# Kernel optimization log

Hardware: AMD Instinct MI355X
Metric: run time of the kernel (lower is better)

The kernel has to match this reference:

```python
import jax, jax.numpy as jnp
import numpy as np

B, C, N, M = 4, 192, 160, 160
HEADS, DH = 4, 32
HID = HEADS * DH
NMEM = 4
SCALE = DH ** -0.5


def setup_inputs() -> dict:
    key = jax.random.key(0)
    ks = jax.random.split(key, 8)
    std = 0.05
    return {
        "x": jax.random.normal(ks[0], (B, C, N, M), jnp.float32),
        "gq": jnp.ones((C,), jnp.float32),
        "gk": jnp.ones((C,), jnp.float32),
        "gv": jnp.ones((C,), jnp.float32),
        "Wq": jax.random.normal(ks[1], (HID, C), jnp.float32) * std,
        "Wk": jax.random.normal(ks[2], (HID, C), jnp.float32) * std,
        "Wv": jax.random.normal(ks[3], (HID, C), jnp.float32) * std,
        "mem_kv": jax.random.normal(ks[4], (2, HEADS, NMEM, DH), jnp.float32),
        "Wo": jax.random.normal(ks[5], (C, HID), jnp.float32) * std,
        "bo": jnp.zeros((C,), jnp.float32),
        "Wr": jax.random.normal(ks[6], (C, 2 * C), jnp.float32) * std,
    }


def _rms(x, g):
    # lucidrains RMSNorm over channel axis 1: F.normalize(x, dim=1) * g * sqrt(dim)
    n = jnp.sqrt(jnp.sum(x * x, axis=1, keepdims=True))
    gshape = (1, -1) + (1,) * (x.ndim - 2)
    return x / jnp.maximum(n, 1e-12) * g.reshape(gshape) * jnp.sqrt(jnp.asarray(x.shape[1], x.dtype))


def _axial_attn(q_ft, k_ft, v_map, rep, Wq, Wk, Wv, mem_kv, Wo, bo, gq, gk, gv):
    # q_ft: (b, c, Lq) compact queries (spatial (1,Lq) in the original)
    # k_ft: (b, c, Lk) compact keys; original repeats them `rep` times -> (Lk*rep) keys
    # v_map: (b, c, Lk, rep) values (full map, not broadcast)
    # Exact math of softmax over [NMEM + Lk*rep] keys, exploiting the rep-fold
    # duplicated key scores so attn(key i, copy j) has identical weight p_i:
    #   out = sum_mem p_j mem_v_j + sum_i p_i * (sum_rep v[i, r])
    b = q_ft.shape[0]
    q = jnp.einsum('hdc,bcq->bhqd', Wq.reshape(HEADS, DH, -1), _rms(q_ft, gq))
    k = jnp.einsum('hdc,bck->bhkd', Wk.reshape(HEADS, DH, -1), _rms(k_ft, gk))
    v = jnp.einsum('hdc,bckr->bhkrd', Wv.reshape(HEADS, DH, -1), _rms(v_map, gv))
    v_sum = v.sum(axis=3)  # (b,h,Lk,d)
    mem_k, mem_v = mem_kv[0], mem_kv[1]
    s_k = jnp.einsum('bhqd,bhkd->bhqk', q, k) * SCALE      # (b,h,Lq,Lk)
    s_m = jnp.einsum('bhqd,hjd->bhqj', q, mem_k) * SCALE   # (b,h,Lq,NMEM)
    mx = jnp.maximum(s_k.max(-1), s_m.max(-1))             # (b,h,Lq)
    e_k = jnp.exp(s_k - mx[..., None])
    e_m = jnp.exp(s_m - mx[..., None])
    Z = e_m.sum(-1) + rep * e_k.sum(-1)                    # rep copies of each key
    out = (jnp.einsum('bhqj,hjd->bhqd', e_m, mem_v)
           + jnp.einsum('bhqk,bhkd->bhqd', e_k, v_sum)) / Z[..., None]
    out = out.transpose(0, 2, 1, 3).reshape(b, -1, HID)    # (b,Lq,hid), (h d) channel order
    return jnp.einsum('ck,bqk->bcq', Wo, out) + bo[None, :, None]  # (b,c,Lq)


def reference(x, gq, gk, gv, Wq, Wk, Wv, mem_kv, Wo, bo, Wr):
    # x: (b,c,n,m); mask=None path
    row_ft = x.mean(axis=3)  # (b,c,n)
    col_ft = x.mean(axis=2)  # (b,c,m)
    # row attention: n queries, keys = col_ft repeated n times, values = x^T (spatial (m,n))
    row_attn = _axial_attn(row_ft, col_ft, x.transpose(0, 1, 3, 2), N,
                           Wq, Wk, Wv, mem_kv, Wo, bo, gq, gk, gv)  # (b,c,n)
    # col attention (shared weights): m queries, keys = row_ft repeated m times, values = x
    col_attn = _axial_attn(col_ft, row_ft, x, M,
                           Wq, Wk, Wv, mem_kv, Wo, bo, gq, gk, gv)  # (b,c,m)
    # broadcast to (b,c,n,m), concat on channels, 1x1 conv reduce (bias=False)
    Wr1, Wr2 = Wr[:, :C], Wr[:, C:]
    out = (jnp.einsum('dc,bcn->bdn', Wr1, row_attn)[:, :, :, None]
           + jnp.einsum('dc,bcm->bdm', Wr2, col_attn)[:, :, None, :])
    return out
```

## Files before the change

kernel.cpp:

```cpp
#include <hip/hip_runtime.h>
#include <math.h>

constexpr int B_ = 4, C_ = 192, N_ = 160, M_ = 160;
constexpr int NM_ = N_ * M_;
constexpr float SQRT_C = 13.856406460551018f;
constexpr float SCALE_ = 0.17677669529663687f;

__device__ __forceinline__ float wred_sum(float v) {
    #pragma unroll
    for (int o = 32; o > 0; o >>= 1) v += __shfl_xor(v, o, 64);
    return v;
}
__device__ __forceinline__ float wred_max(float v) {
    #pragma unroll
    for (int o = 32; o > 0; o >>= 1) v = fmaxf(v, __shfl_xor(v, o, 64));
    return v;
}

__global__ void prep_kernel(const float* __restrict__ Wr, const float* __restrict__ Wo,
                            const float* __restrict__ bo,
                            const float* __restrict__ Wq, const float* __restrict__ Wk,
                            const float* __restrict__ Wv, const float* __restrict__ gq,
                            const float* __restrict__ gk, const float* __restrict__ gv,
                            float* __restrict__ WfT, float* __restrict__ bfb,
                            float* __restrict__ WT) {
    int bx = blockIdx.x, tid = threadIdx.x;
    if (bx < 192) {
        int sub = tid >> 7, hd = tid & 127;
        int pair = bx * 2 + sub;
        int t = pair / 192, dch = pair % 192;
        const float* wr = Wr + dch * 384 + t * 192;
        float acc = 0.f;
        for (int c = 0; c < 192; c++) acc += wr[c] * Wo[c * 128 + hd];
        WfT[hd * 384 + pair] = acc;
        if (hd == 0) {
            float s = 0.f;
            for (int c = 0; c < 192; c++) s += wr[c] * bo[c];
            bfb[pair] = s;
        }
    } else {
        int g = (bx - 192) * 256 + tid;
        int mat = g / 24576, r2 = g % 24576;
        int c = r2 >> 7, hd = r2 & 127;
        const float* W = (mat == 0) ? Wq : ((mat == 1) ? Wk : Wv);
        const float* gv_ = (mat == 0) ? gq : ((mat == 1) ? gk : gv);
        WT[g] = gv_[c] * W[hd * 192 + c];
    }
}

__global__ void ssq_part_kernel(const float* __restrict__ x, float* __restrict__ psum) {
    int bx = blockIdx.x;
    int chunk = bx / 400, blk = bx % 400;
    int g = blk * 256 + threadIdx.x;
    int b = g / NM_, nm = g - b * NM_;
    const float* xp = x + ((size_t)(b * C_ + chunk * 32)) * NM_ + nm;
    float ssq = 0.f;
    #pragma unroll
    for (int cc = 0; cc < 32; cc++) { float v = xp[(size_t)cc * NM_]; ssq += v * v; }
    psum[chunk * (B_ * NM_) + g] = ssq;
}

__global__ void rnorm_kernel(const float* __restrict__ psum, float* __restrict__ rn) {
    int g = blockIdx.x * 256 + threadIdx.x;
    float s = 0.f;
    #pragma unroll
    for (int ch = 0; ch < 6; ch++) s += psum[ch * (B_ * NM_) + g];
    rn[g] = SQRT_C / fmaxf(sqrtf(s), 1e-12f);
}

__global__ void rowcol_kernel(const float* __restrict__ x, const float* __restrict__ rn,
                              float* __restrict__ rowft, float* __restrict__ colft,
                              float* __restrict__ Srow, float* __restrict__ Scol) {
    __shared__ float cpart[8][2][160];
    int bc = blockIdx.x;
    int b = bc / C_;
    int tid = threadIdx.x, w = tid >> 6, lane = tid & 63;
    const float* xp = x + (size_t)bc * NM_;
    const float* rp = rn + (size_t)b * NM_;
    int m0 = lane, m1 = lane + 64, m2 = lane + 128;
    bool ok2 = (m2 < M_);
    float cr0 = 0, cr1 = 0, cr2 = 0, cn0 = 0, cn1 = 0, cn2 = 0;
    for (int n = w; n < N_; n += 8) {
        const float* xr = xp + n * M_;
        const float* rr = rp + n * M_;
        float a0 = xr[m0], a1 = xr[m1], a2 = ok2 ? xr[m2] : 0.f;
        float r0 = rr[m0], r1 = rr[m1], r2 = ok2 ? rr[m2] : 0.f;
        float b0 = a0 * r0, b1 = a1 * r1, b2 = a2 * r2;
        cr0 += a0; cr1 += a1; cr2 += a2;
        cn0 += b0; cn1 += b1; cn2 += b2;
        float rs = wred_sum(a0 + a1 + a2);
        float rsn = wred_sum(b0 + b1 + b2);
        if (lane == 0) {
            rowft[bc * N_ + n] = rs * (1.0f / 160.0f);
            Srow[bc * N_ + n] = rsn;
        }
    }
    cpart[w][0][m0] = cr0; cpart[w][0][m1] = cr1; if (ok2) cpart[w][0][m2] = cr2;
    cpart[w][1][m0] = cn0; cpart[w][1][m1] = cn1; if (ok2) cpart[w][1][m2] = cn2;
    __syncthreads();
    if (tid < M_) {
        float sr = 0.f, sn = 0.f;
        #pragma unroll
        for (int ww = 0; ww < 8; ww++) { sr += cpart[ww][0][tid]; sn += cpart[ww][1][tid]; }
        colft[bc * M_ + tid] = sr * (1.0f / 160.0f);
        Scol[bc * M_ + tid] = sn;
    }
}

__global__ void proj_kernel(const float* __restrict__ WT,
                            const float* __restrict__ rowft, const float* __restrict__ colft,
                            const float* __restrict__ Srow, const float* __restrict__ Scol,
                            float* __restrict__ Qb, float* __restrict__ Kb, float* __restrict__ Vb) {
    __shared__ float in_s[192 * 4];
    __shared__ float sc_s[4];
    int bx = blockIdx.x;
    int pt = bx % 40, rest = bx / 40;
    int mat = rest % 3; int r2 = rest / 3;
    int t = r2 % 2, b = r2 / 2;
    const float* src; float* dst;
    if (mat == 0)      { src = (t == 0) ? rowft : colft; dst = Qb; }
    else if (mat == 1) { src = (t == 0) ? colft : rowft; dst = Kb; }
    else               { src = (t == 0) ? Scol  : Srow;  dst = Vb; }
    const float* Wt = WT + mat * 24576;
    int tid = threadIdx.x;
    for (int idx = tid; idx < 192 * 4; idx += 256) {
        int c = idx >> 2, p = idx & 3;
        in_s[idx] = src[(b * C_ + c) * 160 + pt * 4 + p];
    }
    __syncthreads();
    int w = tid >> 6, lane = tid & 63;
    if (mat < 2) {
        float v0 = in_s[lane * 4 + w];
        float v1 = in_s[(lane + 64) * 4 + w];
        float v2 = in_s[(lane + 128) * 4 + w];
        float ssq = wred_sum(v0 * v0 + v1 * v1 + v2 * v2);
        if (lane == 0) sc_s[w] = SQRT_C / fmaxf(sqrtf(ssq), 1e-12f);
    } else {
        if (tid < 4) sc_s[tid] = 1.0f;
    }
    __syncthreads();
    int hd = tid & 127, pc = tid >> 7, p0 = pc * 2;
    float a0 = 0.f, a1 = 0.f;
    for (int c = 0; c < 192; c++) {
        float wv = Wt[c * 128 + hd];
        a0 += wv * in_s[c * 4 + p0];
        a1 += wv * in_s[c * 4 + p0 + 1];
    }
    int posbase = (b * 2 + t) * 160 + pt * 4 + p0;
    dst[(size_t)posbase * 128 + hd]       = a0 * sc_s[p0];
    dst[(size_t)(posbase + 1) * 128 + hd] = a1 * sc_s[p0 + 1];
}

__global__ void attn_kernel(const float* __restrict__ Qb, const float* __restrict__ Kb,
                            const float* __restrict__ Vb, const float* __restrict__ memkv,
                            float* __restrict__ AO) {
    __shared__ float k_s[160 * 33];
    __shared__ float v_s[160 * 33];
    __shared__ float q_s[8 * 33];
    __shared__ float e_s[8 * 160];
    __shared__ float mk[128];
    __shared__ float mv[128];
    int bx = blockIdx.x;
    int qt = bx % 20; int r = bx / 20;
    int h = r & 3; r >>= 2;
    int t = r & 1; int b = r >> 1;
    int tid = threadIdx.x, w = tid >> 6, lane = tid & 63;
    int btbase = ((b * 2 + t) * 160) * 128 + h * 32;
    for (int idx = tid; idx < 160 * 32; idx += 256) {
        int kk = idx >> 5, d = idx & 31;
        k_s[kk * 33 + d] = Kb[btbase + kk * 128 + d];
        v_s[kk * 33 + d] = Vb[btbase + kk * 128 + d];
    }
    { int q = tid >> 5, d = tid & 31;
      q_s[q * 33 + d] = Qb[btbase + (qt * 8 + q) * 128 + d]; }
    if (tid < 128) {
        mk[tid] = memkv[h * 128 + tid];
        mv[tid] = memkv[512 + h * 128 + tid];
    }
    __syncthreads();
    float kr0[32], kr1[32], kr2[32];
    #pragma unroll
    for (int d = 0; d < 32; d++) {
        kr0[d] = k_s[lane * 33 + d];
        kr1[d] = k_s[(lane + 64) * 33 + d];
        kr2[d] = (lane < 32) ? k_s[(lane + 128) * 33 + d] : 0.f;
    }
    float p;
    {
        int pj = lane >> 3, qi = pj >> 2, j = pj & 3;
        int db = (lane & 7) * 4;
        p = 0.f;
        #pragma unroll
        for (int dd = 0; dd < 4; dd++)
            p += q_s[(w * 2 + qi) * 33 + db + dd] * mk[j * 32 + db + dd];
        p += __shfl_xor(p, 1, 64); p += __shfl_xor(p, 2, 64); p += __shfl_xor(p, 4, 64);
        p *= SCALE_;
    }
    float sm[2][4];
    #pragma unroll
    for (int j = 0; j < 4; j++) {
        sm[0][j] = __shfl(p, j * 8, 64);
        sm[1][j] = __shfl(p, 32 + j * 8, 64);
    }
    int dpv = lane & 31;
    float Zq[2], accm[2];
    #pragma unroll
    for (int qi = 0; qi < 2; qi++) {
        int qrow = (w * 2 + qi) * 33;
        float s0 = 0, s1 = 0, s2 = 0;
        #pragma unroll
        for (int d = 0; d < 32; d++) {
            float qv = q_s[qrow + d];
            s0 += qv * kr0[d]; s1 += qv * kr1[d]; s2 += qv * kr2[d];
        }
        s0 *= SCALE_; s1 *= SCALE_;
        s2 = (lane < 32) ? s2 * SCALE_ : -1e30f;
        float mx = fmaxf(fmaxf(s0, s1), s2);
        mx = fmaxf(mx, fmaxf(fmaxf(sm[qi][0], sm[qi][1]), fmaxf(sm[qi][2], sm[qi][3])));
        mx = wred_max(mx);
        float e0 = __expf(s0 - mx), e1 = __expf(s1 - mx);
        float e2 = (lane < 32) ? __expf(s2 - mx) : 0.f;
        int eb = (w * 2 + qi) * 160;
        e_s[eb + lane] = e0; e_s[eb + 64 + lane] = e1;
        if (lane < 32) e_s[eb + 128 + lane] = e2;
        float esum = wred_sum(e0 + e1 + e2);
        float em0 = __expf(sm[qi][0] - mx), em1 = __expf(sm[qi][1] - mx);
        float em2 = __expf(sm[qi][2] - mx), em3 = __expf(sm[qi][3] - mx);
        Zq[qi] = (em0 + em1 + em2 + em3) + 160.0f * esum;
        accm[qi] = em0 * mv[dpv] + em1 * mv[32 + dpv] + em2 * mv[64 + dpv] + em3 * mv[96 + dpv];
    }
    int half = lane >> 5, k0 = half * 80;
    int eb0 = (w * 2) * 160, eb1 = (w * 2 + 1) * 160;
    float a0 = 0, a1 = 0;
    for (int kk = 0; kk < 80; kk++) {
        float v = v_s[(k0 + kk) * 33 + dpv];
        a0 += e_s[eb0 + k0 + kk] * v;
        a1 += e_s[eb1 + k0 + kk] * v;
    }
    a0 += __shfl_down(a0, 32, 64);
    a1 += __shfl_down(a1, 32, 64);
    if (lane < 32) {
        AO[btbase + (qt * 8 + w * 2 + 0) * 128 + lane] = (accm[0] + a0) / Zq[0];
        AO[btbase + (qt * 8 + w * 2 + 1) * 128 + lane] = (accm[1] + a1) / Zq[1];
    }
}

__global__ void oproj_kernel(const float* __restrict__ WfT, const float* __restrict__ bfb,
                             const float* __restrict__ AO, float* __restrict__ Rr,
                             float* __restrict__ Ccv) {
    __shared__ float ao_s[2 * 128];
    int bx = blockIdx.x;
    int pt = bx % 80, rest = bx / 80;
    int t = rest & 1, b = rest >> 1;
    int tid = threadIdx.x;
    for (int idx = tid; idx < 256; idx += 192)
        ao_s[idx] = AO[(size_t)((b * 2 + t) * 160 + pt * 2 + (idx >> 7)) * 128 + (idx & 127)];
    __syncthreads();
    int dch = tid;
    int tofs = t * 192 + dch;
    float a0 = 0.f, a1 = 0.f;
    for (int hd = 0; hd < 128; hd++) {
        float wv = WfT[hd * 384 + tofs];
        a0 += wv * ao_s[hd];
        a1 += wv * ao_s[128 + hd];
    }
    float bb = bfb[tofs];
    float* dst = t ? Ccv : Rr;
    dst[(b * C_ + dch) * 160 + pt * 2 + 0] = a0 + bb;
    dst[(b * C_ + dch) * 160 + pt * 2 + 1] = a1 + bb;
}

__global__ void final_kernel(const float* __restrict__ Rr, const float* __restrict__ Ccv,
                             float* __restrict__ out) {
    __shared__ float Rl[160];
    __shared__ float Cl[160];
    int bd = blockIdx.x;
    int tid = threadIdx.x;
    if (tid < 160) { Rl[tid] = Rr[bd * 160 + tid]; Cl[tid] = Ccv[bd * 160 + tid]; }
    __syncthreads();
    float* base = out + (size_t)bd * NM_;
    for (int idx = tid; idx < 160 * 40; idx += 256) {
        int n = idx / 40, m4 = idx - n * 40;
        float r = Rl[n];
        float4 v;
        v.x = r + Cl[m4 * 4 + 0];
        v.y = r + Cl[m4 * 4 + 1];
        v.z = r + Cl[m4 * 4 + 2];
        v.w = r + Cl[m4 * 4 + 3];
        *reinterpret_cast<float4*>(base + n * 160 + m4 * 4) = v;
    }
}

extern "C" void kernel_launch(void* const* d_in, const int* in_sizes, int n_in,
                              void* d_out, int out_size, void* d_ws, size_t ws_size,
                              hipStream_t stream) {
    const float* x    = (const float*)d_in[0];
    const float* gq   = (const float*)d_in[1];
    const float* gk   = (const float*)d_in[2];
    const float* gv   = (const float*)d_in[3];
    const float* Wq   = (const float*)d_in[4];
    const float* Wk   = (const float*)d_in[5];
    const float* Wv   = (const float*)d_in[6];
    const float* mkv  = (const float*)d_in[7];
    const float* Wo   = (const float*)d_in[8];
    const float* bo   = (const float*)d_in[9];
    const float* Wr   = (const float*)d_in[10];
    float* out = (float*)d_out;

    float* ws = (float*)d_ws;
    float* rn    = ws;
    float* rowft = rn    + 102400;
    float* colft = rowft + 122880;
    float* Srow  = colft + 122880;
    float* Scol  = Srow  + 122880;
    float* WT    = Scol  + 122880;
    float* Qb    = WT    + 73728;
    float* Kb    = Qb    + 163840;
    float* Vb    = Kb    + 163840;
    float* AO    = Vb    + 163840;
    float* Rr    = AO    + 163840;
    float* Ccv   = Rr    + 122880;
    float* WfT   = Ccv   + 122880;
    float* bfb   = WfT   + 49152;
    float* psum  = Qb;

    prep_kernel<<<480, 256, 0, stream>>>(Wr, Wo, bo, Wq, Wk, Wv, gq, gk, gv, WfT, bfb, WT);
    ssq_part_kernel<<<2400, 256, 0, stream>>>(x, psum);
    rnorm_kernel<<<400, 256, 0, stream>>>(psum, rn);
    rowcol_kernel<<<768, 512, 0, stream>>>(x, rn, rowft, colft, Srow, Scol);
    proj_kernel<<<960, 256, 0, stream>>>(WT, rowft, colft, Srow, Scol, Qb, Kb, Vb);
    attn_kernel<<<640, 256, 0, stream>>>(Qb, Kb, Vb, mkv, AO);
    oproj_kernel<<<640, 192, 0, stream>>>(WfT, bfb, AO, Rr, Ccv);
    final_kernel<<<768, 256, 0, stream>>>(Rr, Ccv, out);
}
```

Before: 226.4 us.

## Fuse norm passes into prep kernel and vectorize proj, attention, oproj loads

Merges the weight-prep, partial sum-of-squares and rnorm kernels into one launch in which each thread loops over all 192 channels, removing the psum round trip and two launches. It also changes the WT and WfT layouts to hd-major/pair-major so proj and oproj can read weights as contiguous float4 along the reduction axis. The attention kernel stores V transposed and pads its shared arrays so K, Q, V and e reads become float4. The single-pass norm gives only 400 blocks a long serial dependent loop, which may hide memory latency worse than the old 2400-block split.

```diff
diff --git a/kernel.cpp b/kernel.cpp
--- a/kernel.cpp
+++ b/kernel.cpp
@@ -17,60 +17,50 @@
     return v;
 }
 
-__global__ void prep_kernel(const float* __restrict__ Wr, const float* __restrict__ Wo,
-                            const float* __restrict__ bo,
-                            const float* __restrict__ Wq, const float* __restrict__ Wk,
-                            const float* __restrict__ Wv, const float* __restrict__ gq,
-                            const float* __restrict__ gk, const float* __restrict__ gv,
-                            float* __restrict__ WfT, float* __restrict__ bfb,
-                            float* __restrict__ WT) {
+__global__ __launch_bounds__(256) void prep_rn_kernel(
+        const float* __restrict__ x,
+        const float* __restrict__ Wr, const float* __restrict__ Wo,
+        const float* __restrict__ bo,
+        const float* __restrict__ Wq, const float* __restrict__ Wk,
+        const float* __restrict__ Wv, const float* __restrict__ gq,
+        const float* __restrict__ gk, const float* __restrict__ gv,
+        float* __restrict__ rn, float* __restrict__ WfT2,
+        float* __restrict__ bfb, float* __restrict__ WT) {
     int bx = blockIdx.x, tid = threadIdx.x;
-    if (bx < 192) {
-        int sub = tid >> 7, hd = tid & 127;
-        int pair = bx * 2 + sub;
+    if (bx < 400) {
+        int g = bx * 256 + tid;
+        int b = g / NM_, nm = g - b * NM_;
+        const float* xp = x + (size_t)b * (C_ * NM_) + nm;
+        float s = 0.f;
+        #pragma unroll 16
+        for (int c = 0; c < C_; c++) { float v = xp[(size_t)c * NM_]; s += v * v; }
+        rn[g] = SQRT_C / fmaxf(sqrtf(s), 1e-12f);
+    } else if (bx < 592) {
+        int pair = (bx - 400) * 2 + (tid >> 7);
+        int hd = tid & 127;
         int t = pair / 192, dch = pair % 192;
         const float* wr = Wr + dch * 384 + t * 192;
         float acc = 0.f;
         for (int c = 0; c < 192; c++) acc += wr[c] * Wo[c * 128 + hd];
-        WfT[hd * 384 + pair] = acc;
+        WfT2[pair * 128 + hd] = acc;
         if (hd == 0) {
-            float s = 0.f;
-            for (int c = 0; c < 192; c++) s += wr[c] * bo[c];
-            bfb[pair] = s;
+            float sb = 0.f;
+            for (int c = 0; c < 192; c++) sb += wr[c] * bo[c];
+            bfb[pair] = sb;
         }
     } else {
-        int g = (bx - 192) * 256 + tid;
-        int mat = g / 24576, r2 = g % 24576;
-        int c = r2 >> 7, hd = r2 & 127;
-        const float* W = (mat == 0) ? Wq : ((mat == 1) ? Wk : Wv);
-        const float* gv_ = (mat == 0) ? gq : ((mat == 1) ? gk : gv);
-        WT[g] = gv_[c] * W[hd * 192 + c];
-    }
-}
-
-__global__ void ssq_part_kernel(const float* __restrict__ x, float* __restrict__ psum) {
-    int bx = blockIdx.x;
-    int chunk = bx / 400, blk = bx % 400;
-    int g = blk * 256 + threadIdx.x;
-    int b = g / NM_, nm = g - b * NM_;
-    const float* xp = x + ((size_t)(b * C_ + chunk * 32)) * NM_ + nm;
-    float ssq = 0.f;
-    #pragma unroll
-    for (int cc = 0; cc < 32; cc++) { float v = xp[(size_t)cc * NM_]; ssq += v * v; }
-    psum[chunk * (B_ * NM_) + g] = ssq;
-}
-
-__global__ void rnorm_kernel(const float* __restrict__ psum, float* __restrict__ rn) {
-    int g = blockIdx.x * 256 + threadIdx.x;
-    float s = 0.f;
-    #pragma unroll
-    for (int ch = 0; ch < 6; ch++) s += psum[ch * (B_ * NM_) + g];
-    rn[g] = SQRT_C / fmaxf(sqrtf(s), 1e-12f);
-}
-
-__global__ void rowcol_kernel(const float* __restrict__ x, const float* __restrict__ rn,
-                              float* __restrict__ rowft, float* __restrict__ colft,
-                              float* __restrict__ Srow, float* __restrict__ Scol) {
+        int g = (bx - 592) * 256 + tid;
+        int mat = g / 24576, r2 = g - mat * 24576;
+        const float* W  = (mat == 0) ? Wq : ((mat == 1) ? Wk : Wv);
+        const float* gp = (mat == 0) ? gq : ((mat == 1) ? gk : gv);
+        WT[g] = gp[r2 % 192] * W[r2];
+    }
+}
+
+__global__ __launch_bounds__(512) void rowcol_kernel(
+        const float* __restrict__ x, const float* __restrict__ rn,
+        float* __restrict__ rowft, float* __restrict__ colft,
+        float* __restrict__ Srow, float* __restrict__ Scol) {
     __shared__ float cpart[8][2][160];
     int bc = blockIdx.x;
     int b = bc / C_;
@@ -107,11 +97,12 @@
     }
 }
 
-__global__ void proj_kernel(const float* __restrict__ WT,
-                            const float* __restrict__ rowft, const float* __restrict__ colft,
-                            const float* __restrict__ Srow, const float* __restrict__ Scol,
-                            float* __restrict__ Qb, float* __restrict__ Kb, float* __restrict__ Vb) {
-    __shared__ float in_s[192 * 4];
+__global__ __launch_bounds__(256) void proj_kernel(
+        const float* __restrict__ WT,
+        const float* __restrict__ rowft, const float* __restrict__ colft,
+        const float* __restrict__ Srow, const float* __restrict__ Scol,
+        float* __restrict__ Qb, float* __restrict__ Kb, float* __restrict__ Vb) {
+    __shared__ float in_s[4 * 196];
     __shared__ float sc_s[4];
     int bx = blockIdx.x;
     int pt = bx % 40, rest = bx / 40;
@@ -123,40 +114,47 @@
     else               { src = (t == 0) ? Scol  : Srow;  dst = Vb; }
     const float* Wt = WT + mat * 24576;
     int tid = threadIdx.x;
-    for (int idx = tid; idx < 192 * 4; idx += 256) {
+    for (int idx = tid; idx < 768; idx += 256) {
         int c = idx >> 2, p = idx & 3;
-        in_s[idx] = src[(b * C_ + c) * 160 + pt * 4 + p];
+        in_s[p * 196 + c] = src[(b * C_ + c) * 160 + pt * 4 + p];
     }
     __syncthreads();
     int w = tid >> 6, lane = tid & 63;
     if (mat < 2) {
-        float v0 = in_s[lane * 4 + w];
-        float v1 = in_s[(lane + 64) * 4 + w];
-        float v2 = in_s[(lane + 128) * 4 + w];
+        float v0 = in_s[w * 196 + lane];
+        float v1 = in_s[w * 196 + lane + 64];
+        float v2 = in_s[w * 196 + lane + 128];
         float ssq = wred_sum(v0 * v0 + v1 * v1 + v2 * v2);
         if (lane == 0) sc_s[w] = SQRT_C / fmaxf(sqrtf(ssq), 1e-12f);
     } else {
         if (tid < 4) sc_s[tid] = 1.0f;
     }
     __syncthreads();
-    int hd = tid & 127, pc = tid >> 7, p0 = pc * 2;
+    int hd = tid & 127, p0 = (tid >> 7) * 2;
+    const float* wp = Wt + hd * 192;
+    const float* i0p = &in_s[p0 * 196];
+    const float* i1p = &in_s[(p0 + 1) * 196];
     float a0 = 0.f, a1 = 0.f;
-    for (int c = 0; c < 192; c++) {
-        float wv = Wt[c * 128 + hd];
-        a0 += wv * in_s[c * 4 + p0];
-        a1 += wv * in_s[c * 4 + p0 + 1];
+    #pragma unroll 4
+    for (int c0 = 0; c0 < 192; c0 += 4) {
+        float4 wv = *reinterpret_cast<const float4*>(wp + c0);
+        float4 u0 = *reinterpret_cast<const float4*>(i0p + c0);
+        float4 u1 = *reinterpret_cast<const float4*>(i1p + c0);
+        a0 += wv.x * u0.x + wv.y * u0.y + wv.z * u0.z + wv.w * u0.w;
+        a1 += wv.x * u1.x + wv.y * u1.y + wv.z * u1.z + wv.w * u1.w;
     }
     int posbase = (b * 2 + t) * 160 + pt * 4 + p0;
     dst[(size_t)posbase * 128 + hd]       = a0 * sc_s[p0];
     dst[(size_t)(posbase + 1) * 128 + hd] = a1 * sc_s[p0 + 1];
 }
 
-__global__ void attn_kernel(const float* __restrict__ Qb, const float* __restrict__ Kb,
-                            const float* __restrict__ Vb, const float* __restrict__ memkv,
-                            float* __restrict__ AO) {
-    __shared__ float k_s[160 * 33];
-    __shared__ float v_s[160 * 33];
-    __shared__ float q_s[8 * 33];
+__global__ __launch_bounds__(256) void attn_kernel(
+        const float* __restrict__ Qb, const float* __restrict__ Kb,
+        const float* __restrict__ Vb, const float* __restrict__ memkv,
+        float* __restrict__ AO) {
+    __shared__ float k_s[160 * 36];
+    __shared__ float v_s[32 * 172];
+    __shared__ float q_s[8 * 36];
     __shared__ float e_s[8 * 160];
     __shared__ float mk[128];
     __shared__ float mv[128];
@@ -166,33 +164,41 @@
     int t = r & 1; int b = r >> 1;
     int tid = threadIdx.x, w = tid >> 6, lane = tid & 63;
     int btbase = ((b * 2 + t) * 160) * 128 + h * 32;
-    for (int idx = tid; idx < 160 * 32; idx += 256) {
-        int kk = idx >> 5, d = idx & 31;
-        k_s[kk * 33 + d] = Kb[btbase + kk * 128 + d];
-        v_s[kk * 33 + d] = Vb[btbase + kk * 128 + d];
-    }
-    { int q = tid >> 5, d = tid & 31;
-      q_s[q * 33 + d] = Qb[btbase + (qt * 8 + q) * 128 + d]; }
+    for (int idx = tid; idx < 1280; idx += 256) {
+        int k = idx >> 3, dq = idx & 7;
+        float4 kv = *reinterpret_cast<const float4*>(Kb + btbase + k * 128 + dq * 4);
+        *reinterpret_cast<float4*>(&k_s[k * 36 + dq * 4]) = kv;
+        float4 vv = *reinterpret_cast<const float4*>(Vb + btbase + k * 128 + dq * 4);
+        v_s[(dq * 4 + 0) * 172 + k] = vv.x;
+        v_s[(dq * 4 + 1) * 172 + k] = vv.y;
+        v_s[(dq * 4 + 2) * 172 + k] = vv.z;
+        v_s[(dq * 4 + 3) * 172 + k] = vv.w;
+    }
+    if (tid < 64) {
+        int q = tid >> 3, dq = tid & 7;
+        *reinterpret_cast<float4*>(&q_s[q * 36 + dq * 4]) =
+            *reinterpret_cast<const float4*>(Qb + btbase + (qt * 8 + q) * 128 + dq * 4);
+    }
     if (tid < 128) {
         mk[tid] = memkv[h * 128 + tid];
         mv[tid] = memkv[512 + h * 128 + tid];
     }
     __syncthreads();
-    float kr0[32], kr1[32], kr2[32];
-    #pragma unroll
-    for (int d = 0; d < 32; d++) {
-        kr0[d] = k_s[lane * 33 + d];
-        kr1[d] = k_s[(lane + 64) * 33 + d];
-        kr2[d] = (lane < 32) ? k_s[(lane + 128) * 33 + d] : 0.f;
+    float4 kr0[8], kr1[8], kr2[8];
+    #pragma unroll
+    for (int dq = 0; dq < 8; dq++) {
+        kr0[dq] = *reinterpret_cast<const float4*>(&k_s[lane * 36 + dq * 4]);
+        kr1[dq] = *reinterpret_cast<const float4*>(&k_s[(lane + 64) * 36 + dq * 4]);
+        if (lane < 32) kr2[dq] = *reinterpret_cast<const float4*>(&k_s[(lane + 128) * 36 + dq * 4]);
+        else           kr2[dq] = make_float4(0.f, 0.f, 0.f, 0.f);
     }
     float p;
     {
         int pj = lane >> 3, qi = pj >> 2, j = pj & 3;
         int db = (lane & 7) * 4;
-        p = 0.f;
-        #pragma unroll
-        for (int dd = 0; dd < 4; dd++)
-            p += q_s[(w * 2 + qi) * 33 + db + dd] * mk[j * 32 + db + dd];
+        float4 qv = *reinterpret_cast<const float4*>(&q_s[(w * 2 + qi) * 36 + db]);
+        float4 mkv = *reinterpret_cast<const float4*>(&mk[j * 32 + db]);
+        p = qv.x * mkv.x + qv.y * mkv.y + qv.z * mkv.z + qv.w * mkv.w;
         p += __shfl_xor(p, 1, 64); p += __shfl_xor(p, 2, 64); p += __shfl_xor(p, 4, 64);
         p *= SCALE_;
     }
@@ -206,12 +212,14 @@
     float Zq[2], accm[2];
     #pragma unroll
     for (int qi = 0; qi < 2; qi++) {
-        int qrow = (w * 2 + qi) * 33;
-        float s0 = 0, s1 = 0, s2 = 0;
+        const float* qrow = &q_s[(w * 2 + qi) * 36];
+        float s0 = 0.f, s1 = 0.f, s2 = 0.f;
         #pragma unroll
-        for (int d = 0; d < 32; d++) {
-            float qv = q_s[qrow + d];
-            s0 += qv * kr0[d]; s1 += qv * kr1[d]; s2 += qv * kr2[d];
+        for (int dq = 0; dq < 8; dq++) {
+            float4 qv = *reinterpret_cast<const float4*>(qrow + dq * 4);
+            s0 += qv.x * kr0[dq].x + qv.y * kr0[dq].y + qv.z * kr0[dq].z + qv.w * kr0[dq].w;
+            s1 += qv.x * kr1[dq].x + qv.y * kr1[dq].y + qv.z * kr1[dq].z + qv.w * kr1[dq].w;
+            s2 += qv.x * kr2[dq].x + qv.y * kr2[dq].y + qv.z * kr2[dq].z + qv.w * kr2[dq].w;
         }
         s0 *= SCALE_; s1 *= SCALE_;
         s2 = (lane < 32) ? s2 * SCALE_ : -1e30f;
@@ -230,12 +238,17 @@
         accm[qi] = em0 * mv[dpv] + em1 * mv[32 + dpv] + em2 * mv[64 + dpv] + em3 * mv[96 + dpv];
     }
     int half = lane >> 5, k0 = half * 80;
-    int eb0 = (w * 2) * 160, eb1 = (w * 2 + 1) * 160;
-    float a0 = 0, a1 = 0;
-    for (int kk = 0; kk < 80; kk++) {
-        float v = v_s[(k0 + kk) * 33 + dpv];
-        a0 += e_s[eb0 + k0 + kk] * v;
-        a1 += e_s[eb1 + k0 + kk] * v;
+    const float* vrow = &v_s[dpv * 172 + k0];
+    const float* e0p = &e_s[(w * 2) * 160 + k0];
+    const float* e1p = &e_s[(w * 2 + 1) * 160 + k0];
+    float a0 = 0.f, a1 = 0.f;
+    #pragma unroll 4
+    for (int kk = 0; kk < 80; kk += 4) {
+        float4 vv = *reinterpret_cast<const float4*>(vrow + kk);
+        float4 e0 = *reinterpret_cast<const float4*>(e0p + kk);
+        float4 e1 = *reinterpret_cast<const float4*>(e1p + kk);
+        a0 += e0.x * vv.x + e0.y * vv.y + e0.z * vv.z + e0.w * vv.w;
+        a1 += e1.x * vv.x + e1.y * vv.y + e1.z * vv.z + e1.w * vv.w;
     }
     a0 += __shfl_down(a0, 32, 64);
     a1 += __shfl_down(a1, 32, 64);
@@ -245,9 +258,10 @@
     }
 }
 
-__global__ void oproj_kernel(const float* __restrict__ WfT, const float* __restrict__ bfb,
-                             const float* __restrict__ AO, float* __restrict__ Rr,
-                             float* __restrict__ Ccv) {
+__global__ __launch_bounds__(192) void oproj_kernel(
+        const float* __restrict__ WfT2, const float* __restrict__ bfb,
+        const float* __restrict__ AO, float* __restrict__ Rr,
+        float* __restrict__ Ccv) {
     __shared__ float ao_s[2 * 128];
     int bx = blockIdx.x;
     int pt = bx % 80, rest = bx / 80;
@@ -256,22 +270,26 @@
     for (int idx = tid; idx < 256; idx += 192)
         ao_s[idx] = AO[(size_t)((b * 2 + t) * 160 + pt * 2 + (idx >> 7)) * 128 + (idx & 127)];
     __syncthreads();
-    int dch = tid;
-    int tofs = t * 192 + dch;
+    int tofs = t * 192 + tid;
+    const float* wp = WfT2 + tofs * 128;
     float a0 = 0.f, a1 = 0.f;
-    for (int hd = 0; hd < 128; hd++) {
-        float wv = WfT[hd * 384 + tofs];
-        a0 += wv * ao_s[hd];
-        a1 += wv * ao_s[128 + hd];
+    #pragma unroll 8
+    for (int hd = 0; hd < 128; hd += 4) {
+        float4 w4 = *reinterpret_cast<const float4*>(wp + hd);
+        float4 x0 = *reinterpret_cast<const float4*>(&ao_s[hd]);
+        float4 x1 = *reinterpret_cast<const float4*>(&ao_s[128 + hd]);
+        a0 += w4.x * x0.x + w4.y * x0.y + w4.z * x0.z + w4.w * x0.w;
+        a1 += w4.x * x1.x + w4.y * x1.y + w4.z * x1.z + w4.w * x1.w;
     }
     float bb = bfb[tofs];
     float* dst = t ? Ccv : Rr;
-    dst[(b * C_ + dch) * 160 + pt * 2 + 0] = a0 + bb;
-    dst[(b * C_ + dch) * 160 + pt * 2 + 1] = a1 + bb;
-}
-
-__global__ void final_kernel(const float* __restrict__ Rr, const float* __restrict__ Ccv,
-                             float* __restrict__ out) {
+    dst[(b * C_ + tid) * 160 + pt * 2 + 0] = a0 + bb;
+    dst[(b * C_ + tid) * 160 + pt * 2 + 1] = a1 + bb;
+}
+
+__global__ __launch_bounds__(256) void final_kernel(
+        const float* __restrict__ Rr, const float* __restrict__ Ccv,
+        float* __restrict__ out) {
     __shared__ float Rl[160];
     __shared__ float Cl[160];
     int bd = blockIdx.x;
@@ -322,11 +340,9 @@
     float* Ccv   = Rr    + 122880;
     float* WfT   = Ccv   + 122880;
     float* bfb   = WfT   + 49152;
-    float* psum  = Qb;
-
-    prep_kernel<<<480, 256, 0, stream>>>(Wr, Wo, bo, Wq, Wk, Wv, gq, gk, gv, WfT, bfb, WT);
-    ssq_part_kernel<<<2400, 256, 0, stream>>>(x, psum);
-    rnorm_kernel<<<400, 256, 0, stream>>>(psum, rn);
+
+    prep_rn_kernel<<<880, 256, 0, stream>>>(x, Wr, Wo, bo, Wq, Wk, Wv, gq, gk, gv,
+                                            rn, WfT, bfb, WT);
     rowcol_kernel<<<768, 512, 0, stream>>>(x, rn, rowft, colft, Srow, Scol);
     proj_kernel<<<960, 256, 0, stream>>>(WT, rowft, colft, Srow, Scol, Qb, Kb, Vb);
     attn_kernel<<<640, 256, 0, stream>>>(Qb, Kb, Vb, mkv, AO);
```

Result: no change. 226.6 us (+0.1%).
